# Performance work log

Measured on AMD Instinct MI355X. Metric: run time of the kernel, lower is better.

Reference implementation:

```python
import jax, jax.numpy as jnp
import numpy as np

NOT_EPSILON = 1.0
B, Q, K, T = 2, 512, 512, 256  # batch, num queries, num keys, dims


def swishmax(x, axis):
    # x * exp(x - max) / (sum(|x * exp(x - max)|) + 1)
    xexp = x * jnp.exp(x - jnp.max(x, axis=axis, keepdims=True))
    return xexp / (jnp.sum(jnp.abs(xexp), axis=axis, keepdims=True) + NOT_EPSILON)


def setup_inputs() -> dict:
    key = jax.random.key(0)
    ks = jax.random.split(key, 8)
    s = 1.0 / np.sqrt(T)
    return {
        "query_tokens": jax.random.normal(ks[0], (B, Q, T), jnp.float32),
        "key_tokens": jax.random.normal(ks[1], (B, K, T), jnp.float32),
        "value_tokens": jax.random.normal(ks[2], (B, K, T), jnp.float32),
        "Wk": jax.random.normal(ks[3], (T, T), jnp.float32) * s,
        "Wq": jax.random.normal(ks[4], (T, T), jnp.float32) * s,
        "Wva": jax.random.normal(ks[5], (T, T), jnp.float32) * s,
        "Wal": jax.random.normal(ks[6], (T, T), jnp.float32) * s,
        "Wvo": jax.random.normal(ks[7], (T, T), jnp.float32) * s,
    }


def reference(query_tokens, key_tokens, value_tokens, Wk, Wq, Wva, Wal, Wvo):
    # torch nn.Linear: y = x @ W.T (no biases)
    k = jnp.einsum('bkt,ut->bku', key_tokens, Wk)      # [B,K,T]
    q = jnp.einsum('bqt,ut->bqu', query_tokens, Wq)    # [B,Q,T]
    # elementwise outer product over token pairs: [B,K,Q,T]
    raw = k[:, :, None, :] * q[:, None, :, :]
    logits = jnp.einsum('bkqt,ut->bkqu', raw, Wal)     # [B,K,Q,T]
    scale = swishmax(logits, axis=-2)                  # normalize over Q
    v = jnp.einsum('bkt,ut->bku', value_tokens, Wva)   # [B,K,T]
    values_scaled = v[:, :, None, :] * scale           # [B,K,Q,T]
    value_sum = values_scaled.sum(axis=-3)             # sum over K -> [B,Q,T]
    return jnp.einsum('bqt,ut->bqu', value_sum, Wvo)   # [B,Q,T]
```

## Files before the change

kernel.cpp:

```cpp
#include <hip/hip_runtime.h>
#include <cstdint>


typedef short bf16x8 __attribute__((ext_vector_type(8)));
typedef float f32x4  __attribute__((ext_vector_type(4)));

__device__ inline float bf2f(short s) {
  return __uint_as_float(((unsigned)(unsigned short)s) << 16);
}
__device__ inline unsigned packrn(float lo, float hi) {
  return __builtin_amdgcn_perm(__float_as_uint(hi) + 0x8000u,
                               __float_as_uint(lo) + 0x8000u, 0x07060302u);
}
__device__ inline unsigned encM(float f) {
  unsigned k = (unsigned)__float_as_int(f);
  return (k & 0x80000000u) ? ~k : (k | 0x80000000u);
}
__device__ inline float decM(unsigned k) {
  int i = (k & 0x80000000u) ? (int)(k ^ 0x80000000u) : (int)~k;
  return __int_as_float(i);
}

#define GEMM_BODY32(X, W, K0, K1)                                               \
  __shared__ __align__(16) float As[16][36];                                    \
  __shared__ __align__(16) float Ws[16][68];                                    \
  const int tid = threadIdx.x;                                                  \
  const int tx4 = (tid & 15) * 4;                                               \
  const int ty2 = (tid >> 4) * 2;                                               \
  const int m0 = blockIdx.x * 32, u0 = blockIdx.y * 64;                         \
  const int lmi = tid >> 2, lc4 = (tid & 3) * 4;                                \
  const bool hasA = tid < 128;                                                  \
  float4 xa, wb;                                                                \
  if (hasA) xa = *(const float4*)&(X)[(size_t)(m0 + lmi) * 256 + (K0) + lc4];   \
  wb = *(const float4*)&(W)[(size_t)(u0 + lmi) * 256 + (K0) + lc4];             \
  float c[2][4] = {};                                                           \
  _Pragma("unroll 1")                                                           \
  for (int t0 = (K0); t0 < (K1); t0 += 16) {                                    \
    __syncthreads();                                                            \
    if (hasA) {                                                                 \
      As[lc4 + 0][lmi] = xa.x; As[lc4 + 1][lmi] = xa.y;                         \
      As[lc4 + 2][lmi] = xa.z; As[lc4 + 3][lmi] = xa.w;                         \
    }                                                                           \
    Ws[lc4 + 0][lmi] = wb.x; Ws[lc4 + 1][lmi] = wb.y;                           \
    Ws[lc4 + 2][lmi] = wb.z; Ws[lc4 + 3][lmi] = wb.w;                           \
    __syncthreads();                                                            \
    if (t0 + 16 < (K1)) {                                                       \
      if (hasA) xa = *(const float4*)&(X)[(size_t)(m0 + lmi) * 256 + t0 + 16 + lc4]; \
      wb = *(const float4*)&(W)[(size_t)(u0 + lmi) * 256 + t0 + 16 + lc4];      \
    }                                                                           \
    _Pragma("unroll")                                                           \
    for (int t = 0; t < 16; ++t) {                                              \
      const float2 a = *(const float2*)&As[t][ty2];                             \
      const float4 w = *(const float4*)&Ws[t][tx4];                             \
      c[0][0] += a.x*w.x; c[0][1] += a.x*w.y; c[0][2] += a.x*w.z; c[0][3] += a.x*w.w; \
      c[1][0] += a.y*w.x; c[1][1] += a.y*w.y; c[1][2] += a.y*w.z; c[1][3] += a.y*w.w; \
    }                                                                           \
  }

__global__ __launch_bounds__(256) void proj3(
    const float* __restrict__ key, const float* __restrict__ value,
    const float* __restrict__ query, const float* __restrict__ Wk,
    const float* __restrict__ Wq, const float* __restrict__ Wva,
    const float* __restrict__ Wal, float* __restrict__ kproj,
    float* __restrict__ vproj, short* __restrict__ qpF,
    short* __restrict__ WalF, float* __restrict__ vsum,
    float* __restrict__ outz)
{
  const int z = blockIdx.z;
  if (z == 3) {
    const int p = blockIdx.x * 4 + blockIdx.y;
    if (p >= 64) return;
    const int t256 = threadIdx.x;
#pragma unroll
    for (int e = 0; e < 4; ++e) {
      const int d = p * 1024 + t256 * 4 + e;
      const int j = d & 7, uu = (d >> 3) & 31, c8g = d >> 8;
      const int ucx = c8g >> 5, cc = c8g & 31;
      const float v = Wal[(ucx * 32 + uu) * 256 + cc * 8 + j];
      WalF[d] = (short)packrn(v, v);
    }
    float4* vz = (float4*)(vsum + p * 4096);
    float4* oz = (float4*)(outz + p * 4096);
#pragma unroll
    for (int e = 0; e < 4; ++e) {
      vz[t256 * 4 + e] = make_float4(0.f, 0.f, 0.f, 0.f);
      oz[t256 * 4 + e] = make_float4(0.f, 0.f, 0.f, 0.f);
    }
    return;
  }
  const float* X = (z == 0) ? key : (z == 1) ? value : query;
  const float* W = (z == 0) ? Wk  : (z == 1) ? Wva   : Wq;
  GEMM_BODY32(X, W, 0, 256);
  if (z == 2) {
    const int tbase = u0 + tx4;
    const int ks = tbase >> 5, l4f = (tbase & 31) >> 3, j0 = tbase & 7;
#pragma unroll
    for (int i = 0; i < 2; ++i) {
      const int m = m0 + ty2 + i;
      const int bb = m >> 9, q = m & 511;
      const int g = q >> 4, l15q = q & 15;
      const size_t idx = ((size_t)(((bb * 32 + g) * 8 + ks) * 64) + l4f * 16 + l15q) * 8 + j0;
      uint2 s; s.x = packrn(c[i][0], c[i][1]); s.y = packrn(c[i][2], c[i][3]);
      *(uint2*)&qpF[idx] = s;
    }
  } else {
    float* C = (z == 0) ? kproj : vproj;
#pragma unroll
    for (int i = 0; i < 2; ++i)
      *(float4*)&C[(size_t)(m0 + ty2 + i) * 256 + u0 + tx4] =
          make_float4(c[i][0], c[i][1], c[i][2], c[i][3]);
  }
}

__global__ __launch_bounds__(256) void gemm_out(
    const float* __restrict__ X, const float* __restrict__ W, float* __restrict__ out)
{
  const int kh = blockIdx.z * 128;
  GEMM_BODY32(X, W, kh, kh + 128);
#pragma unroll
  for (int i = 0; i < 2; ++i)
#pragma unroll
    for (int j = 0; j < 4; ++j)
      atomicAdd(&out[(size_t)(m0 + ty2 + i) * 256 + u0 + tx4 + j], c[i][j]);
}

union Frag { bf16x8 v; unsigned u[4]; };

__global__ __launch_bounds__(512, 2) void kernelC(
    const short* __restrict__ qpF, const float* __restrict__ kproj,
    const float* __restrict__ vproj, const short* __restrict__ WalF,
    float* __restrict__ vsum)
{
  __shared__ __align__(16) short W2F[2][8192];
  __shared__ float vpS[32 * 33];
  __shared__ unsigned statM[96];
  __shared__ float statS[96];

  const int kt = blockIdx.x, uc = blockIdx.y, b = blockIdx.z;
  const int u0 = uc * 32, k0 = kt * 32;
  const int tid = threadIdx.x;
  const int lane = tid & 63, w = tid >> 6;
  const int l15 = lane & 15, l4 = lane >> 4;
  const int uu = tid & 31, c8 = tid >> 5;

  if (tid < 96) { statM[tid] = 0u; statS[tid] = 0.f; }
  {
    const int kk = tid >> 4, uu2 = (tid & 15) * 2;
    const float2 v2 = *(const float2*)&vproj[(size_t)(b * 512 + k0 + kk) * 256 + u0 + uu2];
    vpS[kk * 33 + uu2] = v2.x; vpS[kk * 33 + uu2 + 1] = v2.y;
  }

  float wl0[8], wl1[8];
  {
    const bf16x8 w0 = *(const bf16x8*)&WalF[((size_t)(uc * 32 + c8) * 32 + uu) * 8];
    const bf16x8 w1 = *(const bf16x8*)&WalF[((size_t)(uc * 32 + c8 + 16) * 32 + uu) * 8];
#pragma unroll
    for (int j = 0; j < 8; ++j) { wl0[j] = bf2f(w0[j]); wl1[j] = bf2f(w1[j]); }
  }

  const short* qbase = qpF + (size_t)b * 131072;
  Frag qa[4][8];
#pragma unroll
  for (int qg = 0; qg < 4; ++qg)
#pragma unroll
    for (int ks = 0; ks < 8; ++ks) {
      qa[qg][ks].v = *(const bf16x8*)&qbase[(((size_t)(w * 4 + qg) * 8 + ks) * 64 + lane) * 8];
      asm volatile("" : "+v"(qa[qg][ks].u[0]), "+v"(qa[qg][ks].u[1]),
                        "+v"(qa[qg][ks].u[2]), "+v"(qa[qg][ks].u[3]));
    }

  const int fb = (l4 * 32 + l15) * 8;
  const float* kq = &kproj[(long)(b * 512 + k0) * 256 + c8 * 8];

  {
    const f32x4 a0 = *(const f32x4*)(kq);
    const f32x4 a1 = *(const f32x4*)(kq + 4);
    const f32x4 b0 = *(const f32x4*)(kq + 128);
    const f32x4 b1 = *(const f32x4*)(kq + 132);
    uint4 st;
    st.x = packrn(wl0[0] * a0[0], wl0[1] * a0[1]);
    st.y = packrn(wl0[2] * a0[2], wl0[3] * a0[3]);
    st.z = packrn(wl0[4] * a1[0], wl0[5] * a1[1]);
    st.w = packrn(wl0[6] * a1[2], wl0[7] * a1[3]);
    *(uint4*)&W2F[0][(c8 * 32 + uu) * 8] = st;
    st.x = packrn(wl1[0] * b0[0], wl1[1] * b0[1]);
    st.y = packrn(wl1[2] * b0[2], wl1[3] * b0[3]);
    st.z = packrn(wl1[4] * b1[0], wl1[5] * b1[1]);
    st.w = packrn(wl1[6] * b1[2], wl1[7] * b1[3]);
    *(uint4*)&W2F[0][((c8 + 16) * 32 + uu) * 8] = st;
  }
  __syncthreads();

  const f32x4 z4 = {0.f, 0.f, 0.f, 0.f};
  f32x4 acc[4][2] = {z4, z4, z4, z4, z4, z4, z4, z4};

#pragma unroll 1
  for (int kk = 0; kk < 32; ++kk) {
    const int cs = kk & 1, ss = kk % 3;

    f32x4 a0, a1, b0, b1;
    if (kk < 31) {
      const float* kn = kq + (size_t)(kk + 1) * 256;
      a0 = *(const f32x4*)(kn);
      a1 = *(const f32x4*)(kn + 4);
      b0 = *(const f32x4*)(kn + 128);
      b1 = *(const f32x4*)(kn + 132);
    }

    f32x4 lg[4][2] = {z4, z4, z4, z4, z4, z4, z4, z4};
#pragma unroll
    for (int ks = 0; ks < 8; ++ks) {
      const bf16x8 f0 = *(const bf16x8*)&W2F[cs][fb + ks * 1024];
      const bf16x8 f1 = *(const bf16x8*)&W2F[cs][fb + ks * 1024 + 128];
#pragma unroll
      for (int qg = 0; qg < 4; ++qg) {
        lg[qg][0] = __builtin_amdgcn_mfma_f32_16x16x32_bf16(qa[qg][ks].v, f0, lg[qg][0], 0, 0, 0);
        lg[qg][1] = __builtin_amdgcn_mfma_f32_16x16x32_bf16(qa[qg][ks].v, f1, lg[qg][1], 0, 0, 0);
      }
    }
#pragma unroll
    for (int qg = 0; qg < 4; ++qg)
      asm volatile("" : "+v"(lg[qg][0]), "+v"(lg[qg][1]));

    if (kk < 31) {
      uint4 st;
      st.x = packrn(wl0[0] * a0[0], wl0[1] * a0[1]);
      st.y = packrn(wl0[2] * a0[2], wl0[3] * a0[3]);
      st.z = packrn(wl0[4] * a1[0], wl0[5] * a1[1]);
      st.w = packrn(wl0[6] * a1[2], wl0[7] * a1[3]);
      *(uint4*)&W2F[cs ^ 1][(c8 * 32 + uu) * 8] = st;
      st.x = packrn(wl1[0] * b0[0], wl1[1] * b0[1]);
      st.y = packrn(wl1[2] * b0[2], wl1[3] * b0[3]);
      st.z = packrn(wl1[4] * b1[0], wl1[5] * b1[1]);
      st.w = packrn(wl1[6] * b1[2], wl1[7] * b1[3]);
      *(uint4*)&W2F[cs ^ 1][((c8 + 16) * 32 + uu) * 8] = st;
    }

    float Mv[2], Sv[2];
#pragma unroll
    for (int ug = 0; ug < 2; ++ug) {
      const float m0q = fmaxf(fmaxf(lg[0][ug][0], lg[0][ug][1]), fmaxf(lg[0][ug][2], lg[0][ug][3]));
      const float m1q = fmaxf(fmaxf(lg[1][ug][0], lg[1][ug][1]), fmaxf(lg[1][ug][2], lg[1][ug][3]));
      const float m2q = fmaxf(fmaxf(lg[2][ug][0], lg[2][ug][1]), fmaxf(lg[2][ug][2], lg[2][ug][3]));
      const float m3q = fmaxf(fmaxf(lg[3][ug][0], lg[3][ug][1]), fmaxf(lg[3][ug][2], lg[3][ug][3]));
      float m = fmaxf(fmaxf(m0q, m1q), fmaxf(m2q, m3q));
      float sq[4];
#pragma unroll
      for (int qg = 0; qg < 4; ++qg) {
        float p0 = lg[qg][ug][0] * __expf(lg[qg][ug][0]);
        float p1 = lg[qg][ug][1] * __expf(lg[qg][ug][1]);
        float p2 = lg[qg][ug][2] * __expf(lg[qg][ug][2]);
        float p3 = lg[qg][ug][3] * __expf(lg[qg][ug][3]);
        lg[qg][ug][0] = p0; lg[qg][ug][1] = p1;
        lg[qg][ug][2] = p2; lg[qg][ug][3] = p3;
        sq[qg] = (fabsf(p0) + fabsf(p1)) + (fabsf(p2) + fabsf(p3));
      }
      float s = (sq[0] + sq[1]) + (sq[2] + sq[3]);
      m = fmaxf(m, __shfl_xor(m, 16));
      m = fmaxf(m, __shfl_xor(m, 32));
      s += __shfl_xor(s, 16);
      s += __shfl_xor(s, 32);
      Mv[ug] = m; Sv[ug] = s;
    }
    if (l4 == 0) {
      atomicMax(&statM[ss * 32 + l15],      encM(Mv[0]));
      atomicMax(&statM[ss * 32 + 16 + l15], encM(Mv[1]));
      atomicAdd(&statS[ss * 32 + l15],      Sv[0]);
      atomicAdd(&statS[ss * 32 + 16 + l15], Sv[1]);
    }
    __syncthreads();

#pragma unroll
    for (int ug = 0; ug < 2; ++ug) {
      const int ui = ug * 16 + l15;
      const float M = decM(statM[ss * 32 + ui]);
      const float S = statS[ss * 32 + ui];
      const float em = __expf(-M);
      const float g = vpS[kk * 33 + ui] * em * __builtin_amdgcn_rcpf(fmaf(S, em, 1.0f));
#pragma unroll
      for (int qg = 0; qg < 4; ++qg)
#pragma unroll
        for (int i = 0; i < 4; ++i)
          acc[qg][ug][i] = fmaf(g, lg[qg][ug][i], acc[qg][ug][i]);
    }
#pragma unroll
    for (int qg = 0; qg < 4; ++qg)
      asm volatile("" : "+v"(acc[qg][0]), "+v"(acc[qg][1]));

    const int rs = (kk + 2) % 3;
    if (tid < 32) { statM[rs * 32 + tid] = 0u; statS[rs * 32 + tid] = 0.f; }
  }

#pragma unroll
  for (int qg = 0; qg < 4; ++qg)
#pragma unroll
    for (int ug = 0; ug < 2; ++ug)
#pragma unroll
      for (int i = 0; i < 4; ++i)
        atomicAdd(&vsum[(size_t)(b * 512 + w * 64 + qg * 16 + l4 * 4 + i) * 256 +
                        u0 + ug * 16 + l15],
                  acc[qg][ug][i]);
}

extern "C" void kernel_launch(void* const* d_in, const int* in_sizes, int n_in,
                              void* d_out, int out_size, void* d_ws, size_t ws_size,
                              hipStream_t stream) {
  const float* query = (const float*)d_in[0];
  const float* key   = (const float*)d_in[1];
  const float* value = (const float*)d_in[2];
  const float* Wk    = (const float*)d_in[3];
  const float* Wq    = (const float*)d_in[4];
  const float* Wva   = (const float*)d_in[5];
  const float* Wal   = (const float*)d_in[6];
  const float* Wvo   = (const float*)d_in[7];
  float* ws = (float*)d_ws;

  float* kproj = ws;
  float* vproj = kproj + 262144;
  float* vsum  = vproj + 262144;
  short* qpF   = (short*)(vsum + 262144);
  short* WalF  = qpF + 262144;
  float* out   = (float*)d_out;

  proj3<<<dim3(32, 4, 4), 256, 0, stream>>>(key, value, query, Wk, Wq, Wva, Wal,
                                            kproj, vproj, qpF, WalF, vsum, out);
  kernelC<<<dim3(16, 8, 2), 512, 0, stream>>>(qpF, kproj, vproj, WalF, vsum);
  gemm_out<<<dim3(32, 4, 2), 256, 0, stream>>>(vsum, Wvo, out);
}
```

Measured before the change: 191.9 us.

## Fuse three kernels into one cooperative kernel with grid syncs

Merges the projection, the main swishmax/MFMA kernel and the output GEMM into a single cooperative launch of 256 blocks of 512 threads. Each block runs two virtual 256-thread GEMM tiles in the first and last phases, with grid.sync separating the phases. This removes two kernel launches and the gaps between them. The cost is grid-wide barriers, and the launch requires all 256 blocks to be co-resident. The output GEMM is now split four ways along K instead of two, which adds atomics.

Measured after the change: 285.1 us. 48.6% more time.

```diff
diff --git a/kernel.cpp b/kernel.cpp
--- a/kernel.cpp
+++ b/kernel.cpp
@@ -1,5 +1,8 @@
 #include <hip/hip_runtime.h>
+#include <hip/hip_cooperative_groups.h>
 #include <cstdint>
+
+namespace cg = cooperative_groups;
 
 
 typedef short bf16x8 __attribute__((ext_vector_type(8)));
@@ -21,285 +24,301 @@
   return __int_as_float(i);
 }
 
-#define GEMM_BODY32(X, W, K0, K1)                                               \
-  __shared__ __align__(16) float As[16][36];                                    \
-  __shared__ __align__(16) float Ws[16][68];                                    \
-  const int tid = threadIdx.x;                                                  \
-  const int tx4 = (tid & 15) * 4;                                               \
-  const int ty2 = (tid >> 4) * 2;                                               \
-  const int m0 = blockIdx.x * 32, u0 = blockIdx.y * 64;                         \
-  const int lmi = tid >> 2, lc4 = (tid & 3) * 4;                                \
-  const bool hasA = tid < 128;                                                  \
-  float4 xa, wb;                                                                \
-  if (hasA) xa = *(const float4*)&(X)[(size_t)(m0 + lmi) * 256 + (K0) + lc4];   \
-  wb = *(const float4*)&(W)[(size_t)(u0 + lmi) * 256 + (K0) + lc4];             \
-  float c[2][4] = {};                                                           \
-  _Pragma("unroll 1")                                                           \
-  for (int t0 = (K0); t0 < (K1); t0 += 16) {                                    \
-    __syncthreads();                                                            \
-    if (hasA) {                                                                 \
-      As[lc4 + 0][lmi] = xa.x; As[lc4 + 1][lmi] = xa.y;                         \
-      As[lc4 + 2][lmi] = xa.z; As[lc4 + 3][lmi] = xa.w;                         \
-    }                                                                           \
-    Ws[lc4 + 0][lmi] = wb.x; Ws[lc4 + 1][lmi] = wb.y;                           \
-    Ws[lc4 + 2][lmi] = wb.z; Ws[lc4 + 3][lmi] = wb.w;                           \
-    __syncthreads();                                                            \
-    if (t0 + 16 < (K1)) {                                                       \
-      if (hasA) xa = *(const float4*)&(X)[(size_t)(m0 + lmi) * 256 + t0 + 16 + lc4]; \
-      wb = *(const float4*)&(W)[(size_t)(u0 + lmi) * 256 + t0 + 16 + lc4];      \
-    }                                                                           \
-    _Pragma("unroll")                                                           \
-    for (int t = 0; t < 16; ++t) {                                              \
-      const float2 a = *(const float2*)&As[t][ty2];                             \
-      const float4 w = *(const float4*)&Ws[t][tx4];                             \
-      c[0][0] += a.x*w.x; c[0][1] += a.x*w.y; c[0][2] += a.x*w.z; c[0][3] += a.x*w.w; \
-      c[1][0] += a.y*w.x; c[1][1] += a.y*w.y; c[1][2] += a.y*w.z; c[1][3] += a.y*w.w; \
-    }                                                                           \
+union Frag { bf16x8 v; unsigned u[4]; };
+
+__device__ __forceinline__ void gemm32_body(
+    const float* __restrict__ X, const float* __restrict__ W,
+    float* __restrict__ As, float* __restrict__ Ws,
+    int m0, int u0, int K0, int K1, int t, float c[2][4])
+{
+  const int lmi = t >> 2, lc4 = (t & 3) * 4;
+  const int tx4 = (t & 15) * 4;
+  const int ty2 = (t >> 4) * 2;
+  const bool hasA = t < 128;
+  float4 xa, wb;
+  if (hasA) xa = *(const float4*)&X[(size_t)(m0 + lmi) * 256 + K0 + lc4];
+  wb = *(const float4*)&W[(size_t)(u0 + lmi) * 256 + K0 + lc4];
+#pragma unroll 1
+  for (int t0 = K0; t0 < K1; t0 += 16) {
+    __syncthreads();
+    if (hasA) {
+      As[(lc4 + 0) * 36 + lmi] = xa.x; As[(lc4 + 1) * 36 + lmi] = xa.y;
+      As[(lc4 + 2) * 36 + lmi] = xa.z; As[(lc4 + 3) * 36 + lmi] = xa.w;
+    }
+    Ws[(lc4 + 0) * 68 + lmi] = wb.x; Ws[(lc4 + 1) * 68 + lmi] = wb.y;
+    Ws[(lc4 + 2) * 68 + lmi] = wb.z; Ws[(lc4 + 3) * 68 + lmi] = wb.w;
+    __syncthreads();
+    if (t0 + 16 < K1) {
+      if (hasA) xa = *(const float4*)&X[(size_t)(m0 + lmi) * 256 + t0 + 16 + lc4];
+      wb = *(const float4*)&W[(size_t)(u0 + lmi) * 256 + t0 + 16 + lc4];
+    }
+#pragma unroll
+    for (int tt = 0; tt < 16; ++tt) {
+      const float2 a = *(const float2*)&As[tt * 36 + ty2];
+      const float4 wv = *(const float4*)&Ws[tt * 68 + tx4];
+      c[0][0] += a.x * wv.x; c[0][1] += a.x * wv.y;
+      c[0][2] += a.x * wv.z; c[0][3] += a.x * wv.w;
+      c[1][0] += a.y * wv.x; c[1][1] += a.y * wv.y;
+      c[1][2] += a.y * wv.z; c[1][3] += a.y * wv.w;
+    }
   }
-
-__global__ __launch_bounds__(256) void proj3(
-    const float* __restrict__ key, const float* __restrict__ value,
-    const float* __restrict__ query, const float* __restrict__ Wk,
+}
+
+__global__ __launch_bounds__(512, 2) void fused(
+    const float* __restrict__ query, const float* __restrict__ key,
+    const float* __restrict__ value, const float* __restrict__ Wk,
     const float* __restrict__ Wq, const float* __restrict__ Wva,
-    const float* __restrict__ Wal, float* __restrict__ kproj,
-    float* __restrict__ vproj, short* __restrict__ qpF,
-    short* __restrict__ WalF, float* __restrict__ vsum,
-    float* __restrict__ outz)
+    const float* __restrict__ Wal, const float* __restrict__ Wvo,
+    float* __restrict__ kproj, float* __restrict__ vproj,
+    float* __restrict__ vsum, short* __restrict__ qpF,
+    short* __restrict__ WalF, float* __restrict__ out)
 {
-  const int z = blockIdx.z;
-  if (z == 3) {
-    const int p = blockIdx.x * 4 + blockIdx.y;
-    if (p >= 64) return;
-    const int t256 = threadIdx.x;
-#pragma unroll
-    for (int e = 0; e < 4; ++e) {
-      const int d = p * 1024 + t256 * 4 + e;
-      const int j = d & 7, uu = (d >> 3) & 31, c8g = d >> 8;
-      const int ucx = c8g >> 5, cc = c8g & 31;
-      const float v = Wal[(ucx * 32 + uu) * 256 + cc * 8 + j];
-      WalF[d] = (short)packrn(v, v);
-    }
-    float4* vz = (float4*)(vsum + p * 4096);
-    float4* oz = (float4*)(outz + p * 4096);
-#pragma unroll
-    for (int e = 0; e < 4; ++e) {
-      vz[t256 * 4 + e] = make_float4(0.f, 0.f, 0.f, 0.f);
-      oz[t256 * 4 + e] = make_float4(0.f, 0.f, 0.f, 0.f);
-    }
-    return;
+  __shared__ __align__(16) unsigned char smem[37888];
+  cg::grid_group grid = cg::this_grid();
+  const int bid = blockIdx.x;
+  const int tid = threadIdx.x;
+  const int half = tid >> 8, t = tid & 255;
+  const int vb = bid * 2 + half;
+
+  {
+    float* As = (float*)(smem + half * 6656);
+    float* Ws = (float*)(smem + half * 6656 + 2304);
+    if (vb < 384) {
+      const int z = vb >> 7, r = vb & 127;
+      const int m0 = (r >> 2) * 32, u0 = (r & 3) * 64;
+      const float* X = (z == 0) ? key : (z == 1) ? value : query;
+      const float* Wm = (z == 0) ? Wk : (z == 1) ? Wva : Wq;
+      float c[2][4] = {};
+      gemm32_body(X, Wm, As, Ws, m0, u0, 0, 256, t, c);
+      const int tx4 = (t & 15) * 4, ty2 = (t >> 4) * 2;
+      if (z == 2) {
+        const int tbase = u0 + tx4;
+        const int ks = tbase >> 5, l4f = (tbase & 31) >> 3, j0 = tbase & 7;
+#pragma unroll
+        for (int i = 0; i < 2; ++i) {
+          const int m = m0 + ty2 + i;
+          const int bb = m >> 9, q = m & 511;
+          const int g = q >> 4, l15q = q & 15;
+          const size_t idx =
+              ((size_t)(((bb * 32 + g) * 8 + ks) * 64) + l4f * 16 + l15q) * 8 + j0;
+          uint2 s; s.x = packrn(c[i][0], c[i][1]); s.y = packrn(c[i][2], c[i][3]);
+          *(uint2*)&qpF[idx] = s;
+        }
+      } else {
+        float* C = (z == 0) ? kproj : vproj;
+#pragma unroll
+        for (int i = 0; i < 2; ++i)
+          *(float4*)&C[(size_t)(m0 + ty2 + i) * 256 + u0 + tx4] =
+              make_float4(c[i][0], c[i][1], c[i][2], c[i][3]);
+      }
+    } else if (vb < 448) {
+      const int p = vb - 384;
+#pragma unroll
+      for (int e = 0; e < 4; ++e) {
+        const int d = p * 1024 + t * 4 + e;
+        const int j = d & 7, uu = (d >> 3) & 31, c8g = d >> 8;
+        const int ucx = c8g >> 5, cc = c8g & 31;
+        const float v = Wal[(ucx * 32 + uu) * 256 + cc * 8 + j];
+        WalF[d] = (short)packrn(v, v);
+      }
+      float4* vz = (float4*)(vsum + p * 4096);
+#pragma unroll
+      for (int e = 0; e < 4; ++e) vz[t * 4 + e] = make_float4(0.f, 0.f, 0.f, 0.f);
+    } else {
+      const int p = vb - 448;
+      float4* oz = (float4*)(out + p * 4096);
+#pragma unroll
+      for (int e = 0; e < 4; ++e) oz[t * 4 + e] = make_float4(0.f, 0.f, 0.f, 0.f);
+    }
   }
-  const float* X = (z == 0) ? key : (z == 1) ? value : query;
-  const float* W = (z == 0) ? Wk  : (z == 1) ? Wva   : Wq;
-  GEMM_BODY32(X, W, 0, 256);
-  if (z == 2) {
-    const int tbase = u0 + tx4;
-    const int ks = tbase >> 5, l4f = (tbase & 31) >> 3, j0 = tbase & 7;
-#pragma unroll
-    for (int i = 0; i < 2; ++i) {
-      const int m = m0 + ty2 + i;
-      const int bb = m >> 9, q = m & 511;
-      const int g = q >> 4, l15q = q & 15;
-      const size_t idx = ((size_t)(((bb * 32 + g) * 8 + ks) * 64) + l4f * 16 + l15q) * 8 + j0;
-      uint2 s; s.x = packrn(c[i][0], c[i][1]); s.y = packrn(c[i][2], c[i][3]);
-      *(uint2*)&qpF[idx] = s;
-    }
-  } else {
-    float* C = (z == 0) ? kproj : vproj;
-#pragma unroll
-    for (int i = 0; i < 2; ++i)
-      *(float4*)&C[(size_t)(m0 + ty2 + i) * 256 + u0 + tx4] =
-          make_float4(c[i][0], c[i][1], c[i][2], c[i][3]);
-  }
-}
-
-__global__ __launch_bounds__(256) void gemm_out(
-    const float* __restrict__ X, const float* __restrict__ W, float* __restrict__ out)
-{
-  const int kh = blockIdx.z * 128;
-  GEMM_BODY32(X, W, kh, kh + 128);
-#pragma unroll
-  for (int i = 0; i < 2; ++i)
-#pragma unroll
-    for (int j = 0; j < 4; ++j)
-      atomicAdd(&out[(size_t)(m0 + ty2 + i) * 256 + u0 + tx4 + j], c[i][j]);
-}
-
-union Frag { bf16x8 v; unsigned u[4]; };
-
-__global__ __launch_bounds__(512, 2) void kernelC(
-    const short* __restrict__ qpF, const float* __restrict__ kproj,
-    const float* __restrict__ vproj, const short* __restrict__ WalF,
-    float* __restrict__ vsum)
-{
-  __shared__ __align__(16) short W2F[2][8192];
-  __shared__ float vpS[32 * 33];
-  __shared__ unsigned statM[96];
-  __shared__ float statS[96];
-
-  const int kt = blockIdx.x, uc = blockIdx.y, b = blockIdx.z;
-  const int u0 = uc * 32, k0 = kt * 32;
-  const int tid = threadIdx.x;
-  const int lane = tid & 63, w = tid >> 6;
-  const int l15 = lane & 15, l4 = lane >> 4;
-  const int uu = tid & 31, c8 = tid >> 5;
-
-  if (tid < 96) { statM[tid] = 0u; statS[tid] = 0.f; }
+  grid.sync();
+
   {
-    const int kk = tid >> 4, uu2 = (tid & 15) * 2;
-    const float2 v2 = *(const float2*)&vproj[(size_t)(b * 512 + k0 + kk) * 256 + u0 + uu2];
-    vpS[kk * 33 + uu2] = v2.x; vpS[kk * 33 + uu2 + 1] = v2.y;
-  }
-
-  float wl0[8], wl1[8];
-  {
-    const bf16x8 w0 = *(const bf16x8*)&WalF[((size_t)(uc * 32 + c8) * 32 + uu) * 8];
-    const bf16x8 w1 = *(const bf16x8*)&WalF[((size_t)(uc * 32 + c8 + 16) * 32 + uu) * 8];
-#pragma unroll
-    for (int j = 0; j < 8; ++j) { wl0[j] = bf2f(w0[j]); wl1[j] = bf2f(w1[j]); }
-  }
-
-  const short* qbase = qpF + (size_t)b * 131072;
-  Frag qa[4][8];
-#pragma unroll
-  for (int qg = 0; qg < 4; ++qg)
-#pragma unroll
-    for (int ks = 0; ks < 8; ++ks) {
-      qa[qg][ks].v = *(const bf16x8*)&qbase[(((size_t)(w * 4 + qg) * 8 + ks) * 64 + lane) * 8];
-      asm volatile("" : "+v"(qa[qg][ks].u[0]), "+v"(qa[qg][ks].u[1]),
-                        "+v"(qa[qg][ks].u[2]), "+v"(qa[qg][ks].u[3]));
-    }
-
-  const int fb = (l4 * 32 + l15) * 8;
-  const float* kq = &kproj[(long)(b * 512 + k0) * 256 + c8 * 8];
-
-  {
-    const f32x4 a0 = *(const f32x4*)(kq);
-    const f32x4 a1 = *(const f32x4*)(kq + 4);
-    const f32x4 b0 = *(const f32x4*)(kq + 128);
-    const f32x4 b1 = *(const f32x4*)(kq + 132);
-    uint4 st;
-    st.x = packrn(wl0[0] * a0[0], wl0[1] * a0[1]);
-    st.y = packrn(wl0[2] * a0[2], wl0[3] * a0[3]);
-    st.z = packrn(wl0[4] * a1[0], wl0[5] * a1[1]);
-    st.w = packrn(wl0[6] * a1[2], wl0[7] * a1[3]);
-    *(uint4*)&W2F[0][(c8 * 32 + uu) * 8] = st;
-    st.x = packrn(wl1[0] * b0[0], wl1[1] * b0[1]);
-    st.y = packrn(wl1[2] * b0[2], wl1[3] * b0[3]);
-    st.z = packrn(wl1[4] * b1[0], wl1[5] * b1[1]);
-    st.w = packrn(wl1[6] * b1[2], wl1[7] * b1[3]);
-    *(uint4*)&W2F[0][((c8 + 16) * 32 + uu) * 8] = st;
-  }
-  __syncthreads();
-
-  const f32x4 z4 = {0.f, 0.f, 0.f, 0.f};
-  f32x4 acc[4][2] = {z4, z4, z4, z4, z4, z4, z4, z4};
-
-#pragma unroll 1
-  for (int kk = 0; kk < 32; ++kk) {
-    const int cs = kk & 1, ss = kk % 3;
-
-    f32x4 a0, a1, b0, b1;
-    if (kk < 31) {
-      const float* kn = kq + (size_t)(kk + 1) * 256;
-      a0 = *(const f32x4*)(kn);
-      a1 = *(const f32x4*)(kn + 4);
-      b0 = *(const f32x4*)(kn + 128);
-      b1 = *(const f32x4*)(kn + 132);
-    }
-
-    f32x4 lg[4][2] = {z4, z4, z4, z4, z4, z4, z4, z4};
-#pragma unroll
-    for (int ks = 0; ks < 8; ++ks) {
-      const bf16x8 f0 = *(const bf16x8*)&W2F[cs][fb + ks * 1024];
-      const bf16x8 f1 = *(const bf16x8*)&W2F[cs][fb + ks * 1024 + 128];
-#pragma unroll
-      for (int qg = 0; qg < 4; ++qg) {
-        lg[qg][0] = __builtin_amdgcn_mfma_f32_16x16x32_bf16(qa[qg][ks].v, f0, lg[qg][0], 0, 0, 0);
-        lg[qg][1] = __builtin_amdgcn_mfma_f32_16x16x32_bf16(qa[qg][ks].v, f1, lg[qg][1], 0, 0, 0);
-      }
-    }
+    short* W2Fp = (short*)smem;
+    float* vpS = (float*)(smem + 32768);
+    unsigned* statM = (unsigned*)(smem + 36992);
+    float* statS = (float*)(smem + 37376);
+
+    const int kt = bid & 15, uc = (bid >> 4) & 7, b = bid >> 7;
+    const int u0 = uc * 32, k0 = kt * 32;
+    const int lane = tid & 63, w = tid >> 6;
+    const int l15 = lane & 15, l4 = lane >> 4;
+    const int uu = tid & 31, c8 = tid >> 5;
+
+    if (tid < 96) { statM[tid] = 0u; statS[tid] = 0.f; }
+    {
+      const int kk = tid >> 4, uu2 = (tid & 15) * 2;
+      const float2 v2 = *(const float2*)&vproj[(size_t)(b * 512 + k0 + kk) * 256 + u0 + uu2];
+      vpS[kk * 33 + uu2] = v2.x; vpS[kk * 33 + uu2 + 1] = v2.y;
+    }
+
+    float wl0[8], wl1[8];
+    {
+      const bf16x8 w0 = *(const bf16x8*)&WalF[((size_t)(uc * 32 + c8) * 32 + uu) * 8];
+      const bf16x8 w1 = *(const bf16x8*)&WalF[((size_t)(uc * 32 + c8 + 16) * 32 + uu) * 8];
+#pragma unroll
+      for (int j = 0; j < 8; ++j) { wl0[j] = bf2f(w0[j]); wl1[j] = bf2f(w1[j]); }
+    }
+
+    const short* qbase = qpF + (size_t)b * 131072;
+    Frag qa[4][8];
 #pragma unroll
     for (int qg = 0; qg < 4; ++qg)
-      asm volatile("" : "+v"(lg[qg][0]), "+v"(lg[qg][1]));
-
-    if (kk < 31) {
+#pragma unroll
+      for (int ks = 0; ks < 8; ++ks) {
+        qa[qg][ks].v = *(const bf16x8*)&qbase[(((size_t)(w * 4 + qg) * 8 + ks) * 64 + lane) * 8];
+        asm volatile("" : "+v"(qa[qg][ks].u[0]), "+v"(qa[qg][ks].u[1]),
+                          "+v"(qa[qg][ks].u[2]), "+v"(qa[qg][ks].u[3]));
+      }
+
+    const int fb = (l4 * 32 + l15) * 8;
+    const float* kq = &kproj[(long)(b * 512 + k0) * 256 + c8 * 8];
+
+    {
+      const f32x4 a0 = *(const f32x4*)(kq);
+      const f32x4 a1 = *(const f32x4*)(kq + 4);
+      const f32x4 b0 = *(const f32x4*)(kq + 128);
+      const f32x4 b1 = *(const f32x4*)(kq + 132);
       uint4 st;
       st.x = packrn(wl0[0] * a0[0], wl0[1] * a0[1]);
       st.y = packrn(wl0[2] * a0[2], wl0[3] * a0[3]);
       st.z = packrn(wl0[4] * a1[0], wl0[5] * a1[1]);
       st.w = packrn(wl0[6] * a1[2], wl0[7] * a1[3]);
-      *(uint4*)&W2F[cs ^ 1][(c8 * 32 + uu) * 8] = st;
+      *(uint4*)&W2Fp[(c8 * 32 + uu) * 8] = st;
       st.x = packrn(wl1[0] * b0[0], wl1[1] * b0[1]);
       st.y = packrn(wl1[2] * b0[2], wl1[3] * b0[3]);
       st.z = packrn(wl1[4] * b1[0], wl1[5] * b1[1]);
       st.w = packrn(wl1[6] * b1[2], wl1[7] * b1[3]);
-      *(uint4*)&W2F[cs ^ 1][((c8 + 16) * 32 + uu) * 8] = st;
-    }
-
-    float Mv[2], Sv[2];
-#pragma unroll
-    for (int ug = 0; ug < 2; ++ug) {
-      const float m0q = fmaxf(fmaxf(lg[0][ug][0], lg[0][ug][1]), fmaxf(lg[0][ug][2], lg[0][ug][3]));
-      const float m1q = fmaxf(fmaxf(lg[1][ug][0], lg[1][ug][1]), fmaxf(lg[1][ug][2], lg[1][ug][3]));
-      const float m2q = fmaxf(fmaxf(lg[2][ug][0], lg[2][ug][1]), fmaxf(lg[2][ug][2], lg[2][ug][3]));
-      const float m3q = fmaxf(fmaxf(lg[3][ug][0], lg[3][ug][1]), fmaxf(lg[3][ug][2], lg[3][ug][3]));
-      float m = fmaxf(fmaxf(m0q, m1q), fmaxf(m2q, m3q));
-      float sq[4];
-#pragma unroll
-      for (int qg = 0; qg < 4; ++qg) {
-        float p0 = lg[qg][ug][0] * __expf(lg[qg][ug][0]);
-        float p1 = lg[qg][ug][1] * __expf(lg[qg][ug][1]);
-        float p2 = lg[qg][ug][2] * __expf(lg[qg][ug][2]);
-        float p3 = lg[qg][ug][3] * __expf(lg[qg][ug][3]);
-        lg[qg][ug][0] = p0; lg[qg][ug][1] = p1;
-        lg[qg][ug][2] = p2; lg[qg][ug][3] = p3;
-        sq[qg] = (fabsf(p0) + fabsf(p1)) + (fabsf(p2) + fabsf(p3));
-      }
-      float s = (sq[0] + sq[1]) + (sq[2] + sq[3]);
-      m = fmaxf(m, __shfl_xor(m, 16));
-      m = fmaxf(m, __shfl_xor(m, 32));
-      s += __shfl_xor(s, 16);
-      s += __shfl_xor(s, 32);
-      Mv[ug] = m; Sv[ug] = s;
-    }
-    if (l4 == 0) {
-      atomicMax(&statM[ss * 32 + l15],      encM(Mv[0]));
-      atomicMax(&statM[ss * 32 + 16 + l15], encM(Mv[1]));
-      atomicAdd(&statS[ss * 32 + l15],      Sv[0]);
-      atomicAdd(&statS[ss * 32 + 16 + l15], Sv[1]);
+      *(uint4*)&W2Fp[((c8 + 16) * 32 + uu) * 8] = st;
     }
     __syncthreads();
 
-#pragma unroll
-    for (int ug = 0; ug < 2; ++ug) {
-      const int ui = ug * 16 + l15;
-      const float M = decM(statM[ss * 32 + ui]);
-      const float S = statS[ss * 32 + ui];
-      const float em = __expf(-M);
-      const float g = vpS[kk * 33 + ui] * em * __builtin_amdgcn_rcpf(fmaf(S, em, 1.0f));
+    const f32x4 z4 = {0.f, 0.f, 0.f, 0.f};
+    f32x4 acc[4][2] = {z4, z4, z4, z4, z4, z4, z4, z4};
+
+#pragma unroll 1
+    for (int kk = 0; kk < 32; ++kk) {
+      const int cs = kk & 1, ss = kk % 3;
+
+      f32x4 a0, a1, b0, b1;
+      if (kk < 31) {
+        const float* kn = kq + (size_t)(kk + 1) * 256;
+        a0 = *(const f32x4*)(kn);
+        a1 = *(const f32x4*)(kn + 4);
+        b0 = *(const f32x4*)(kn + 128);
+        b1 = *(const f32x4*)(kn + 132);
+      }
+
+      f32x4 lg[4][2] = {z4, z4, z4, z4, z4, z4, z4, z4};
+#pragma unroll
+      for (int ks = 0; ks < 8; ++ks) {
+        const bf16x8 f0 = *(const bf16x8*)&W2Fp[cs * 8192 + fb + ks * 1024];
+        const bf16x8 f1 = *(const bf16x8*)&W2Fp[cs * 8192 + fb + ks * 1024 + 128];
+#pragma unroll
+        for (int qg = 0; qg < 4; ++qg) {
+          lg[qg][0] = __builtin_amdgcn_mfma_f32_16x16x32_bf16(qa[qg][ks].v, f0, lg[qg][0], 0, 0, 0);
+          lg[qg][1] = __builtin_amdgcn_mfma_f32_16x16x32_bf16(qa[qg][ks].v, f1, lg[qg][1], 0, 0, 0);
+        }
+      }
 #pragma unroll
       for (int qg = 0; qg < 4; ++qg)
+        asm volatile("" : "+v"(lg[qg][0]), "+v"(lg[qg][1]));
+
+      if (kk < 31) {
+        uint4 st;
+        st.x = packrn(wl0[0] * a0[0], wl0[1] * a0[1]);
+        st.y = packrn(wl0[2] * a0[2], wl0[3] * a0[3]);
+        st.z = packrn(wl0[4] * a1[0], wl0[5] * a1[1]);
+        st.w = packrn(wl0[6] * a1[2], wl0[7] * a1[3]);
+        *(uint4*)&W2Fp[(cs ^ 1) * 8192 + (c8 * 32 + uu) * 8] = st;
+        st.x = packrn(wl1[0] * b0[0], wl1[1] * b0[1]);
+        st.y = packrn(wl1[2] * b0[2], wl1[3] * b0[3]);
+        st.z = packrn(wl1[4] * b1[0], wl1[5] * b1[1]);
+        st.w = packrn(wl1[6] * b1[2], wl1[7] * b1[3]);
+        *(uint4*)&W2Fp[(cs ^ 1) * 8192 + ((c8 + 16) * 32 + uu) * 8] = st;
+      }
+
+      float Mv[2], Sv[2];
+#pragma unroll
+      for (int ug = 0; ug < 2; ++ug) {
+        const float m0q = fmaxf(fmaxf(lg[0][ug][0], lg[0][ug][1]), fmaxf(lg[0][ug][2], lg[0][ug][3]));
+        const float m1q = fmaxf(fmaxf(lg[1][ug][0], lg[1][ug][1]), fmaxf(lg[1][ug][2], lg[1][ug][3]));
+        const float m2q = fmaxf(fmaxf(lg[2][ug][0], lg[2][ug][1]), fmaxf(lg[2][ug][2], lg[2][ug][3]));
+        const float m3q = fmaxf(fmaxf(lg[3][ug][0], lg[3][ug][1]), fmaxf(lg[3][ug][2], lg[3][ug][3]));
+        float m = fmaxf(fmaxf(m0q, m1q), fmaxf(m2q, m3q));
+        float sq[4];
+#pragma unroll
+        for (int qg = 0; qg < 4; ++qg) {
+          float p0 = lg[qg][ug][0] * __expf(lg[qg][ug][0]);
+          float p1 = lg[qg][ug][1] * __expf(lg[qg][ug][1]);
+          float p2 = lg[qg][ug][2] * __expf(lg[qg][ug][2]);
+          float p3 = lg[qg][ug][3] * __expf(lg[qg][ug][3]);
+          lg[qg][ug][0] = p0; lg[qg][ug][1] = p1;
+          lg[qg][ug][2] = p2; lg[qg][ug][3] = p3;
+          sq[qg] = (fabsf(p0) + fabsf(p1)) + (fabsf(p2) + fabsf(p3));
+        }
+        float s = (sq[0] + sq[1]) + (sq[2] + sq[3]);
+        m = fmaxf(m, __shfl_xor(m, 16));
+        m = fmaxf(m, __shfl_xor(m, 32));
+        s += __shfl_xor(s, 16);
+        s += __shfl_xor(s, 32);
+        Mv[ug] = m; Sv[ug] = s;
+      }
+      if (l4 == 0) {
+        atomicMax(&statM[ss * 32 + l15],      encM(Mv[0]));
+        atomicMax(&statM[ss * 32 + 16 + l15], encM(Mv[1]));
+        atomicAdd(&statS[ss * 32 + l15],      Sv[0]);
+        atomicAdd(&statS[ss * 32 + 16 + l15], Sv[1]);
+      }
+      __syncthreads();
+
+#pragma unroll
+      for (int ug = 0; ug < 2; ++ug) {
+        const int ui = ug * 16 + l15;
+        const float M = decM(statM[ss * 32 + ui]);
+        const float S = statS[ss * 32 + ui];
+        const float em = __expf(-M);
+        const float g = vpS[kk * 33 + ui] * em * __builtin_amdgcn_rcpf(fmaf(S, em, 1.0f));
+#pragma unroll
+        for (int qg = 0; qg < 4; ++qg)
+#pragma unroll
+          for (int i = 0; i < 4; ++i)
+            acc[qg][ug][i] = fmaf(g, lg[qg][ug][i], acc[qg][ug][i]);
+      }
+#pragma unroll
+      for (int qg = 0; qg < 4; ++qg)
+        asm volatile("" : "+v"(acc[qg][0]), "+v"(acc[qg][1]));
+
+      const int rs = (kk + 2) % 3;
+      if (tid < 32) { statM[rs * 32 + tid] = 0u; statS[rs * 32 + tid] = 0.f; }
+    }
+
+#pragma unroll
+    for (int qg = 0; qg < 4; ++qg)
+#pragma unroll
+      for (int ug = 0; ug < 2; ++ug)
 #pragma unroll
         for (int i = 0; i < 4; ++i)
-          acc[qg][ug][i] = fmaf(g, lg[qg][ug][i], acc[qg][ug][i]);
-    }
-#pragma unroll
-    for (int qg = 0; qg < 4; ++qg)
-      asm volatile("" : "+v"(acc[qg][0]), "+v"(acc[qg][1]));
-
-    const int rs = (kk + 2) % 3;
-    if (tid < 32) { statM[rs * 32 + tid] = 0u; statS[rs * 32 + tid] = 0.f; }
+          atomicAdd(&vsum[(size_t)(b * 512 + w * 64 + qg * 16 + l4 * 4 + i) * 256 +
+                          u0 + ug * 16 + l15],
+                    acc[qg][ug][i]);
   }
-
-#pragma unroll
-  for (int qg = 0; qg < 4; ++qg)
-#pragma unroll
-    for (int ug = 0; ug < 2; ++ug)
-#pragma unroll
-      for (int i = 0; i < 4; ++i)
-        atomicAdd(&vsum[(size_t)(b * 512 + w * 64 + qg * 16 + l4 * 4 + i) * 256 +
-                        u0 + ug * 16 + l15],
-                  acc[qg][ug][i]);
+  grid.sync();
+
+  {
+    float* As = (float*)(smem + half * 6656);
+    float* Ws = (float*)(smem + half * 6656 + 2304);
+    const int mt = vb >> 4, ut = (vb >> 2) & 3, kseg = vb & 3;
+    const int m0 = mt * 32, u0 = ut * 64;
+    float c[2][4] = {};
+    gemm32_body(vsum, Wvo, As, Ws, m0, u0, kseg * 64, kseg * 64 + 64, t, c);
+    const int tx4 = (t & 15) * 4, ty2 = (t >> 4) * 2;
+#pragma unroll
+    for (int i = 0; i < 2; ++i)
+#pragma unroll
+      for (int j = 0; j < 4; ++j)
+        atomicAdd(&out[(size_t)(m0 + ty2 + i) * 256 + u0 + tx4 + j], c[i][j]);
+  }
 }
 
 extern "C" void kernel_launch(void* const* d_in, const int* in_sizes, int n_in,
@@ -322,8 +341,11 @@
   short* WalF  = qpF + 262144;
   float* out   = (float*)d_out;
 
-  proj3<<<dim3(32, 4, 4), 256, 0, stream>>>(key, value, query, Wk, Wq, Wva, Wal,
-                                            kproj, vproj, qpF, WalF, vsum, out);
-  kernelC<<<dim3(16, 8, 2), 512, 0, stream>>>(qpF, kproj, vproj, WalF, vsum);
-  gemm_out<<<dim3(32, 4, 2), 256, 0, stream>>>(vsum, Wvo, out);
-}
+  void* args[] = {
+      (void*)&query, (void*)&key, (void*)&value, (void*)&Wk, (void*)&Wq,
+      (void*)&Wva, (void*)&Wal, (void*)&Wvo,
+      (void*)&kproj, (void*)&vproj, (void*)&vsum, (void*)&qpF, (void*)&WalF,
+      (void*)&out};
+  hipLaunchCooperativeKernel((const void*)fused, dim3(256), dim3(512), args, 0,
+                             stream);
+}
```
